# Performance work log

Hardware: AMD Instinct MI355X
Metric: run time of the kernel (lower is better)

The kernel has to match this reference:

```python
import jax, jax.numpy as jnp
import numpy as np

SOS = 1  # parsed_vocab.index('<SOS>')
D = 1024
V_IN = 8000
V_OUT = 8000


def gru_cell(x, h, W_ih, W_hh, b_ih, b_hh):
    # PyTorch GRU cell: gates ordered [r, z, n]
    gi = x @ W_ih.T + b_ih          # [B, 3D]
    gh = h @ W_hh.T + b_hh          # [B, 3D]
    i_r, i_z, i_n = jnp.split(gi, 3, axis=-1)
    h_r, h_z, h_n = jnp.split(gh, 3, axis=-1)
    r = jax.nn.sigmoid(i_r + h_r)
    z = jax.nn.sigmoid(i_z + h_z)
    n = jnp.tanh(i_n + r * h_n)
    return (1.0 - z) * n + z * h


def setup_inputs() -> dict:
    key = jax.random.key(0)
    ks = jax.random.split(key, 16)
    s = 1.0 / np.sqrt(D)
    f = lambda k, shape: jax.random.uniform(k, shape, jnp.float32, -s, s)
    return {
        "src": jax.random.randint(ks[0], (256, 128), 0, V_IN),
        "tgt": jax.random.randint(ks[1], (128, 128), 0, V_OUT),
        "enc_emb": jax.random.normal(ks[2], (V_IN, D), jnp.float32),
        "enc_W_ih": f(ks[3], (3 * D, D)),
        "enc_W_hh": f(ks[4], (3 * D, D)),
        "enc_b_ih": f(ks[5], (3 * D,)),
        "enc_b_hh": f(ks[6], (3 * D,)),
        "dec_emb": jax.random.normal(ks[7], (V_OUT, D), jnp.float32),
        "dec_W_ih": f(ks[8], (3 * D, D)),
        "dec_W_hh": f(ks[9], (3 * D, D)),
        "dec_b_ih": f(ks[10], (3 * D,)),
        "dec_b_hh": f(ks[11], (3 * D,)),
        "out_W": f(ks[12], (V_OUT, D)),
        "out_b": f(ks[13], (V_OUT,)),
    }


def reference(src, tgt, enc_emb, enc_W_ih, enc_W_hh, enc_b_ih, enc_b_hh,
              dec_emb, dec_W_ih, dec_W_hh, dec_b_ih, dec_b_hh, out_W, out_b):
    B = src.shape[1]
    # ---- Encoder: GRU over src, keep final hidden ----
    xs = enc_emb[src]  # [S_src, B, D]
    h0 = jnp.zeros((B, D), xs.dtype)

    def enc_step(h, x):
        return gru_cell(x, h, enc_W_ih, enc_W_hh, enc_b_ih, enc_b_hh), None

    h_enc, _ = jax.lax.scan(enc_step, h0, xs)

    # ---- Decoder: greedy argmax feedback (eval path, tf_ratio=0) ----
    tok0 = jnp.full((B,), SOS, dtype=src.dtype)

    def dec_step(carry, _):
        h, tok = carry
        x = dec_emb[tok]                                  # [B, D]
        h_new = gru_cell(x, h, dec_W_ih, dec_W_hh, dec_b_ih, dec_b_hh)
        logits = h_new @ out_W.T + out_b                  # [B, V_OUT]
        next_tok = jnp.argmax(logits, axis=-1).astype(tok.dtype)
        return (h_new, next_tok), logits

    target_length = tgt.shape[0]
    _, logits = jax.lax.scan(dec_step, (h_enc, tok0), None, length=target_length)
    return logits  # [S_tgt, B, V_OUT]
```

## Files before the change

kernel.cpp:

```cpp
#include <hip/hip_runtime.h>
#include <math.h>

#define DD    1024
#define BB    128
#define G3    3072
#define VOUT  8000
#define S_SRC 256
#define S_TGT 128
#define SOS   1
#define GRID  768
#define KS_F  4

__device__ __forceinline__ float cload(const float* p) {
    return __hip_atomic_load(p, __ATOMIC_RELAXED, __HIP_MEMORY_SCOPE_AGENT);
}
__device__ __forceinline__ void cstore(float* p, float v) {
    __hip_atomic_store(p, v, __ATOMIC_RELAXED, __HIP_MEMORY_SCOPE_AGENT);
}
__device__ __forceinline__ int cloadi(const int* p) {
    return __hip_atomic_load(p, __ATOMIC_RELAXED, __HIP_MEMORY_SCOPE_AGENT);
}
__device__ __forceinline__ void cstorei(int* p, int v) {
    __hip_atomic_store(p, v, __ATOMIC_RELAXED, __HIP_MEMORY_SCOPE_AGENT);
}

__device__ __forceinline__ void gbar(unsigned* bar) {
    __builtin_amdgcn_s_waitcnt(0);
    __syncthreads();
    if (threadIdx.x == 0) {
        unsigned old = __hip_atomic_fetch_add(bar, 1u, __ATOMIC_RELAXED,
                                              __HIP_MEMORY_SCOPE_AGENT);
        unsigned target = (old / GRID + 1u) * GRID;
        while (__hip_atomic_load(bar, __ATOMIC_RELAXED,
                                 __HIP_MEMORY_SCOPE_AGENT) < target)
            __builtin_amdgcn_s_sleep(1);
    }
    __syncthreads();
}

__global__ __launch_bounds__(256) void k_init(float* __restrict__ h, int* __restrict__ tok,
                                              unsigned* __restrict__ bar) {
    int idx = blockIdx.x * 256 + threadIdx.x;
    if (idx < BB * DD) h[idx] = 0.0f;
    if (idx < BB) tok[idx] = SOS;
    if (idx == 0) bar[0] = 0u;
}

template<bool COHA>
__device__ __forceinline__ void gemm_core(
    float (* __restrict__ As)[132], float (* __restrict__ Bs)[34],
    const float* __restrict__ A0, const float* __restrict__ A1,
    const float* __restrict__ A2, const float* __restrict__ A3,
    const float* __restrict__ Brow, int kbeg, int ntiles,
    float (&acc)[8][2])
{
    const int tid = threadIdx.x;
    const int kq  = (tid & 7) * 4;
    const int r0  = tid >> 3;
    const int tx  = tid & 15, ty = tid >> 4;
    const float* Arow[4] = {A0, A1, A2, A3};

    for (int t = 0; t < ntiles; ++t) {
        const int k0 = kbeg + t * 32;
        #pragma unroll
        for (int p = 0; p < 4; ++p) {
            const float* ap = Arow[p] + k0 + kq;
            float vx, vy, vz, vw;
            if (COHA) {
                vx = cload(ap + 0); vy = cload(ap + 1);
                vz = cload(ap + 2); vw = cload(ap + 3);
            } else {
                float4 v = *reinterpret_cast<const float4*>(ap);
                vx = v.x; vy = v.y; vz = v.z; vw = v.w;
            }
            int m = r0 + p * 32;
            As[kq+0][m] = vx; As[kq+1][m] = vy; As[kq+2][m] = vz; As[kq+3][m] = vw;
        }
        {
            float4 v = *reinterpret_cast<const float4*>(Brow + k0 + kq);
            Bs[kq+0][r0] = v.x; Bs[kq+1][r0] = v.y; Bs[kq+2][r0] = v.z; Bs[kq+3][r0] = v.w;
        }
        __syncthreads();
        #pragma unroll
        for (int k = 0; k < 32; ++k) {
            float a[8];
            #pragma unroll
            for (int i = 0; i < 8; ++i) a[i] = As[k][ty*8 + i];
            float b0 = Bs[k][tx*2 + 0], b1 = Bs[k][tx*2 + 1];
            #pragma unroll
            for (int i = 0; i < 8; ++i) {
                acc[i][0] = fmaf(a[i], b0, acc[i][0]);
                acc[i][1] = fmaf(a[i], b1, acc[i][1]);
            }
        }
        __syncthreads();
    }
}


__global__ __launch_bounds__(256, 3) void k_enc_p(
    const float* __restrict__ emb, const int* __restrict__ src,
    const float* __restrict__ Wih, const float* __restrict__ bih,
    const float* __restrict__ Whh, const float* __restrict__ bhh,
    float* __restrict__ h, float* __restrict__ gh_p,
    float* __restrict__ gi_buf, int CH, unsigned* bar)
{
    __shared__ float As[32][132];
    __shared__ float Bs[32][34];
    const int bid = blockIdx.x, tid = threadIdx.x;
    const int r0 = tid >> 3, tx = tid & 15, ty = tid >> 4;

    for (int s = 0; s < S_SRC; ++s) {
        if ((s & (CH - 1)) == 0) {
            const int cs = bid / 96, nt = bid % 96;
            if (cs < CH) {
                const int* srow = src + (s + cs) * BB;
                const float* A0 = emb + (size_t)srow[r0 +  0] * DD;
                const float* A1 = emb + (size_t)srow[r0 + 32] * DD;
                const float* A2 = emb + (size_t)srow[r0 + 64] * DD;
                const float* A3 = emb + (size_t)srow[r0 + 96] * DD;
                float acc[8][2] = {};
                gemm_core<false>(As, Bs, A0, A1, A2, A3,
                                 Wih + (size_t)(nt*32 + r0) * DD, 0, DD/32, acc);
                float* C = gi_buf + (size_t)cs * (BB * G3);
                #pragma unroll
                for (int i = 0; i < 8; ++i) {
                    int m = ty*8 + i;
                    #pragma unroll
                    for (int j = 0; j < 2; ++j) {
                        int n = nt*32 + tx*2 + j;
                        cstore(&C[(size_t)m * G3 + n], acc[i][j] + bih[n]);
                    }
                }
            }
            gbar(bar);
        }
        {
            const int kh = bid / 96, nt = bid % 96;
            const float* A0 = h + (size_t)(r0 +  0) * DD;
            const float* A1 = h + (size_t)(r0 + 32) * DD;
            const float* A2 = h + (size_t)(r0 + 64) * DD;
            const float* A3 = h + (size_t)(r0 + 96) * DD;
            float acc[8][2] = {};
            gemm_core<true>(As, Bs, A0, A1, A2, A3,
                            Whh + (size_t)(nt*32 + r0) * DD, kh * 128, 4, acc);
            float* C = gh_p + (size_t)kh * (BB * G3);
            #pragma unroll
            for (int i = 0; i < 8; ++i) {
                int m = ty*8 + i;
                cstore(&C[(size_t)m * G3 + nt*32 + tx*2 + 0], acc[i][0]);
                cstore(&C[(size_t)m * G3 + nt*32 + tx*2 + 1], acc[i][1]);
            }
        }
        gbar(bar);
        {
            int idx = bid * 256 + tid;
            if (idx < BB * DD) {
                int b = idx >> 10, d = idx & 1023;
                size_t o = (size_t)b * G3 + d;
                const float* gib = gi_buf + (size_t)(s & (CH-1)) * (BB * G3);
                float ir = cload(&gib[o]), iz = cload(&gib[o + DD]),
                      in_ = cload(&gib[o + 2*DD]);
                float hr = bhh[d], hz = bhh[DD + d], hn = bhh[2*DD + d];
                #pragma unroll
                for (int p = 0; p < 8; ++p) {
                    const float* g = gh_p + (size_t)p * (BB * G3);
                    hr += cload(&g[o]); hz += cload(&g[o + DD]); hn += cload(&g[o + 2*DD]);
                }
                float r = 1.0f / (1.0f + expf(-(ir + hr)));
                float z = 1.0f / (1.0f + expf(-(iz + hz)));
                float n = tanhf(in_ + r * hn);
                float hv = cload(&h[idx]);
                cstore(&h[idx], (1.0f - z) * n + z * hv);
            }
        }
        gbar(bar);
    }
}

__global__ __launch_bounds__(256, 3) void k_dec_p(
    const float* __restrict__ emb,
    const float* __restrict__ Wih, const float* __restrict__ bih,
    const float* __restrict__ Whh, const float* __restrict__ bhh,
    const float* __restrict__ outW, const float* __restrict__ outb,
    float* __restrict__ h, float* __restrict__ g_p,
    float* __restrict__ lg_p, int* __restrict__ tok,
    float* __restrict__ out, int KSL, unsigned* bar)
{
    __shared__ float As[32][132];
    __shared__ float Bs[32][34];
    float* sv = &As[0][0];
    int*   si = (int*)&As[8][0];
    const int bid = blockIdx.x, tid = threadIdx.x;
    const int r0 = tid >> 3, tx = tid & 15, ty = tid >> 4;

    for (int t = 0; t < S_TGT; ++t) {
        {
            const int side = bid / 384;
            const int rem  = bid - side * 384;
            const int kh   = rem / 96, nt = rem % 96;
            float acc[8][2] = {};
            if (side) {
                const float* A0 = h + (size_t)(r0 +  0) * DD;
                const float* A1 = h + (size_t)(r0 + 32) * DD;
                const float* A2 = h + (size_t)(r0 + 64) * DD;
                const float* A3 = h + (size_t)(r0 + 96) * DD;
                gemm_core<true>(As, Bs, A0, A1, A2, A3,
                                Whh + (size_t)(nt*32 + r0) * DD, kh * 256, 8, acc);
            } else {
                const float* A0 = emb + (size_t)cloadi(&tok[r0 +  0]) * DD;
                const float* A1 = emb + (size_t)cloadi(&tok[r0 + 32]) * DD;
                const float* A2 = emb + (size_t)cloadi(&tok[r0 + 64]) * DD;
                const float* A3 = emb + (size_t)cloadi(&tok[r0 + 96]) * DD;
                gemm_core<false>(As, Bs, A0, A1, A2, A3,
                                 Wih + (size_t)(nt*32 + r0) * DD, kh * 256, 8, acc);
            }
            float* C = g_p + (size_t)(side*4 + kh) * (BB * G3);
            #pragma unroll
            for (int i = 0; i < 8; ++i) {
                int m = ty*8 + i;
                cstore(&C[(size_t)m * G3 + nt*32 + tx*2 + 0], acc[i][0]);
                cstore(&C[(size_t)m * G3 + nt*32 + tx*2 + 1], acc[i][1]);
            }
        }
        gbar(bar);
        {
            int idx = bid * 256 + tid;
            if (idx < BB * DD) {
                int b = idx >> 10, d = idx & 1023;
                size_t o = (size_t)b * G3 + d;
                float ir = bih[d], iz = bih[DD + d], in_ = bih[2*DD + d];
                #pragma unroll
                for (int p = 0; p < 4; ++p) {
                    const float* g = g_p + (size_t)p * (BB * G3);
                    ir += cload(&g[o]); iz += cload(&g[o + DD]); in_ += cload(&g[o + 2*DD]);
                }
                float hr = bhh[d], hz = bhh[DD + d], hn = bhh[2*DD + d];
                #pragma unroll
                for (int p = 4; p < 8; ++p) {
                    const float* g = g_p + (size_t)p * (BB * G3);
                    hr += cload(&g[o]); hz += cload(&g[o + DD]); hn += cload(&g[o + 2*DD]);
                }
                float r = 1.0f / (1.0f + expf(-(ir + hr)));
                float z = 1.0f / (1.0f + expf(-(iz + hz)));
                float n = tanhf(in_ + r * hn);
                float hv = cload(&h[idx]);
                cstore(&h[idx], (1.0f - z) * n + z * hv);
            }
        }
        gbar(bar);
        {
            const int kh = bid / 250, nt = bid % 250;
            if (kh < KSL) {
                const int t0 = (32 * kh) / KSL, t1 = (32 * (kh + 1)) / KSL;
                const float* A0 = h + (size_t)(r0 +  0) * DD;
                const float* A1 = h + (size_t)(r0 + 32) * DD;
                const float* A2 = h + (size_t)(r0 + 64) * DD;
                const float* A3 = h + (size_t)(r0 + 96) * DD;
                float acc[8][2] = {};
                gemm_core<true>(As, Bs, A0, A1, A2, A3,
                                outW + (size_t)(nt*32 + r0) * DD, t0 * 32, t1 - t0, acc);
                float* C = lg_p + (size_t)kh * (BB * VOUT);
                #pragma unroll
                for (int i = 0; i < 8; ++i) {
                    int m = ty*8 + i;
                    cstore(&C[(size_t)m * VOUT + nt*32 + tx*2 + 0], acc[i][0]);
                    cstore(&C[(size_t)m * VOUT + nt*32 + tx*2 + 1], acc[i][1]);
                }
            }
        }
        gbar(bar);
        if (bid < BB) {
            const int b = bid;
            const size_t ro = (size_t)b * VOUT;
            float* Ct = out + (size_t)t * (BB * VOUT) + ro;
            float bv = -INFINITY; int bi = 0x7fffffff;
            for (int v = tid * 4; v < VOUT; v += 1024) {
                float4 rr = *reinterpret_cast<const float4*>(outb + v);
                for (int kh = 0; kh < KSL; ++kh) {
                    const float* P = lg_p + (size_t)kh * (BB * VOUT) + ro + v;
                    rr.x += cload(P + 0); rr.y += cload(P + 1);
                    rr.z += cload(P + 2); rr.w += cload(P + 3);
                }
                *reinterpret_cast<float4*>(Ct + v) = rr;
                if (rr.x > bv) { bv = rr.x; bi = v + 0; }
                if (rr.y > bv) { bv = rr.y; bi = v + 1; }
                if (rr.z > bv) { bv = rr.z; bi = v + 2; }
                if (rr.w > bv) { bv = rr.w; bi = v + 3; }
            }
            sv[tid] = bv; si[tid] = bi;
            __syncthreads();
            for (int st = 128; st > 0; st >>= 1) {
                if (tid < st) {
                    if (sv[tid+st] > sv[tid] ||
                        (sv[tid+st] == sv[tid] && si[tid+st] < si[tid])) {
                        sv[tid] = sv[tid+st]; si[tid] = si[tid+st];
                    }
                }
                __syncthreads();
            }
            if (tid == 0) cstorei(&tok[b], si[0]);
        }
        gbar(bar);
    }
}


__global__ __launch_bounds__(256) void k_gi_chunk(
    const float* __restrict__ emb, const int* __restrict__ src_c,
    const float* __restrict__ Wih, const float* __restrict__ bih,
    float* __restrict__ gi_buf)
{
    __shared__ float As[32][132];
    __shared__ float Bs[32][34];
    const int n0    = blockIdx.x * 32;
    const int mbase = blockIdx.y * 128;
    const int tid = threadIdx.x;
    const int r0  = tid >> 3, tx = tid & 15, ty = tid >> 4;

    const float* A[4];
    #pragma unroll
    for (int p = 0; p < 4; ++p)
        A[p] = emb + (size_t)src_c[mbase + r0 + p * 32] * DD;
    float acc[8][2] = {};
    gemm_core<false>(As, Bs, A[0], A[1], A[2], A[3],
                     Wih + (size_t)(n0 + r0) * DD, 0, DD/32, acc);
    #pragma unroll
    for (int i = 0; i < 8; ++i) {
        size_t m = (size_t)(mbase + ty*8 + i);
        #pragma unroll
        for (int j = 0; j < 2; ++j) {
            int n = n0 + tx*2 + j;
            gi_buf[m * G3 + n] = acc[i][j] + bih[n];
        }
    }
}

__global__ __launch_bounds__(256) void k_gates_ks(
    const float* __restrict__ emb, const int* __restrict__ tok,
    const float* __restrict__ h,
    const float* __restrict__ Wih, const float* __restrict__ Whh,
    float* __restrict__ gi_base, float* __restrict__ gh_base,
    int side_base)
{
    __shared__ float As[32][132];
    __shared__ float Bs[32][34];
    const int side = side_base + blockIdx.y;
    const int kh   = blockIdx.z;
    const int kseg = DD / KS_F;
    const float* __restrict__ W = side ? Whh : Wih;
    float* __restrict__ C = (side ? gh_base : gi_base) + (size_t)kh * (BB * G3);

    const int n0  = blockIdx.x * 32;
    const int tid = threadIdx.x;
    const int r0  = tid >> 3, tx = tid & 15, ty = tid >> 4;

    const float* A[4];
    #pragma unroll
    for (int p = 0; p < 4; ++p) {
        int m = r0 + p * 32;
        A[p] = side ? (h + (size_t)m * DD) : (emb + (size_t)tok[m] * DD);
    }
    float acc[8][2] = {};
    gemm_core<false>(As, Bs, A[0], A[1], A[2], A[3],
                     W + (size_t)(n0 + r0) * DD, kh * kseg, kseg / 32, acc);
    #pragma unroll
    for (int i = 0; i < 8; ++i) {
        size_t m = (size_t)(ty*8 + i);
        C[m * G3 + n0 + tx*2 + 0] = acc[i][0];
        C[m * G3 + n0 + tx*2 + 1] = acc[i][1];
    }
}

__global__ __launch_bounds__(256) void k_logits_ks(
    const float* __restrict__ h, const float* __restrict__ W,
    float* __restrict__ p_base)
{
    __shared__ float As[32][132];
    __shared__ float Bs[32][34];
    const int kh   = blockIdx.y;
    const int kseg = DD / 2;
    float* __restrict__ C = p_base + (size_t)kh * (BB * VOUT);

    const int n0  = blockIdx.x * 32;
    const int tid = threadIdx.x;
    const int r0  = tid >> 3, tx = tid & 15, ty = tid >> 4;

    const float* A[4];
    #pragma unroll
    for (int p = 0; p < 4; ++p) A[p] = h + (size_t)(r0 + p * 32) * DD;
    float acc[8][2] = {};
    gemm_core<false>(As, Bs, A[0], A[1], A[2], A[3],
                     W + (size_t)(n0 + r0) * DD, kh * kseg, kseg / 32, acc);
    #pragma unroll
    for (int i = 0; i < 8; ++i) {
        size_t m = (size_t)(ty*8 + i);
        C[m * VOUT + n0 + tx*2 + 0] = acc[i][0];
        C[m * VOUT + n0 + tx*2 + 1] = acc[i][1];
    }
}

__global__ __launch_bounds__(256) void k_update_f(
    const float* __restrict__ gi_base, int ns_i, const float* __restrict__ bih,
    const float* __restrict__ gh_base, int ns_h, const float* __restrict__ bhh,
    float* __restrict__ h)
{
    int idx = blockIdx.x * 256 + threadIdx.x;
    int b = idx >> 10, d = idx & 1023;
    size_t o = (size_t)b * G3 + d;

    float ir = 0.f, iz = 0.f, in_ = 0.f;
    for (int p = 0; p < ns_i; ++p) {
        const float* g = gi_base + (size_t)p * (BB * G3);
        ir += g[o]; iz += g[o + DD]; in_ += g[o + 2*DD];
    }
    if (bih) { ir += bih[d]; iz += bih[DD + d]; in_ += bih[2*DD + d]; }

    float hr = 0.f, hz = 0.f, hn = 0.f;
    for (int p = 0; p < ns_h; ++p) {
        const float* g = gh_base + (size_t)p * (BB * G3);
        hr += g[o]; hz += g[o + DD]; hn += g[o + 2*DD];
    }
    hr += bhh[d]; hz += bhh[DD + d]; hn += bhh[2*DD + d];

    float r = 1.0f / (1.0f + expf(-(ir + hr)));
    float z = 1.0f / (1.0f + expf(-(iz + hz)));
    float n = tanhf(in_ + r * hn);
    float hv = h[idx];
    h[idx] = (1.0f - z) * n + z * hv;
}

__global__ __launch_bounds__(256) void k_argmax_out(
    const float* __restrict__ p0, const float* __restrict__ p1,
    const float* __restrict__ bias,
    float* __restrict__ outC, int* __restrict__ tok)
{
    const int b = blockIdx.x;
    const size_t ro = (size_t)b * VOUT;
    const int tid = threadIdx.x;

    float bv = -INFINITY; int bi = 0x7fffffff;
    for (int v = tid * 4; v < VOUT; v += 1024) {
        float4 a = *reinterpret_cast<const float4*>(p0 + ro + v);
        float4 c = *reinterpret_cast<const float4*>(p1 + ro + v);
        float4 bb = *reinterpret_cast<const float4*>(bias + v);
        float4 r;
        r.x = a.x + c.x + bb.x;
        r.y = a.y + c.y + bb.y;
        r.z = a.z + c.z + bb.z;
        r.w = a.w + c.w + bb.w;
        *reinterpret_cast<float4*>(outC + ro + v) = r;
        if (r.x > bv) { bv = r.x; bi = v + 0; }
        if (r.y > bv) { bv = r.y; bi = v + 1; }
        if (r.z > bv) { bv = r.z; bi = v + 2; }
        if (r.w > bv) { bv = r.w; bi = v + 3; }
    }
    __shared__ float sv[256];
    __shared__ int   si[256];
    sv[tid] = bv; si[tid] = bi;
    __syncthreads();
    for (int s = 128; s > 0; s >>= 1) {
        if (tid < s) {
            if (sv[tid+s] > sv[tid] || (sv[tid+s] == sv[tid] && si[tid+s] < si[tid])) {
                sv[tid] = sv[tid+s]; si[tid] = si[tid+s];
            }
        }
        __syncthreads();
    }
    if (tid == 0) tok[b] = si[0];
}

extern "C" void kernel_launch(void* const* d_in, const int* in_sizes, int n_in,
                              void* d_out, int out_size, void* d_ws, size_t ws_size,
                              hipStream_t stream) {
    const int*   src     = (const int*)  d_in[0];
    const float* enc_emb = (const float*)d_in[2];
    const float* eWih    = (const float*)d_in[3];
    const float* eWhh    = (const float*)d_in[4];
    const float* ebih    = (const float*)d_in[5];
    const float* ebhh    = (const float*)d_in[6];
    const float* dec_emb = (const float*)d_in[7];
    const float* dWih    = (const float*)d_in[8];
    const float* dWhh    = (const float*)d_in[9];
    const float* dbih    = (const float*)d_in[10];
    const float* dbhh    = (const float*)d_in[11];
    const float* outW    = (const float*)d_in[12];
    const float* outb    = (const float*)d_in[13];
    float* out = (float*)d_out;

    float* h    = (float*)d_ws;
    float* g_p  = h + BB * DD;
    int*  tok   = (int*)(g_p + 8 * BB * G3);
    unsigned* bar = (unsigned*)(tok + 128);
    float* scratch = (float*)(tok + 256);

    size_t fixed = (size_t)((char*)scratch - (char*)d_ws);
    size_t avail = (ws_size > fixed) ? ws_size - fixed : 0;
    int KSLv = (avail >= (size_t)3 * BB * VOUT * 4) ? 3 : 2;
    int CH = 8;
    while (CH > 1 && (size_t)CH * BB * G3 * 4 > avail) CH >>= 1;

    float* gi_buf = scratch;
    float* lg_p   = scratch;

    static int persist_ok = -1;
    if (persist_ok < 0) {
        int nb_e = 0, nb_d = 0, ncu = 0, dev = 0;
        hipError_t e0 = hipGetDevice(&dev);
        hipError_t e1 = hipOccupancyMaxActiveBlocksPerMultiprocessor(
            &nb_e, (const void*)k_enc_p, 256, 0);
        hipError_t e2 = hipOccupancyMaxActiveBlocksPerMultiprocessor(
            &nb_d, (const void*)k_dec_p, 256, 0);
        hipError_t e3 = hipDeviceGetAttribute(
            &ncu, hipDeviceAttributeMultiprocessorCount, dev);
        persist_ok = (e0 == hipSuccess && e1 == hipSuccess && e2 == hipSuccess &&
                      e3 == hipSuccess && nb_e >= 3 && nb_d >= 3 &&
                      (long)ncu * 3 >= GRID) ? 1 : 0;
    }

    k_init<<<512, 256, 0, stream>>>(h, tok, bar);

    if (persist_ok == 1) {
        k_enc_p<<<GRID, 256, 0, stream>>>(enc_emb, src, eWih, ebih, eWhh, ebhh,
                                          h, g_p, gi_buf, CH, bar);
        k_dec_p<<<GRID, 256, 0, stream>>>(dec_emb, dWih, dbih, dWhh, dbhh,
                                          outW, outb, h, g_p, lg_p, tok,
                                          out, KSLv, bar);
    } else {
        float* gi_p = g_p;
        float* gh_p = g_p + 4 * BB * G3;
        float* p0   = scratch;
        float* p1   = scratch + BB * VOUT;

        for (int c = 0; c < S_SRC; c += CH) {
            k_gi_chunk<<<dim3(96, CH), 256, 0, stream>>>(enc_emb, src + c * BB,
                                                         eWih, ebih, gi_buf);
            for (int s = 0; s < CH; ++s) {
                k_gates_ks<<<dim3(96, 1, KS_F), 256, 0, stream>>>(
                    enc_emb, tok, h, eWih, eWhh, nullptr, gh_p, 1);
                k_update_f<<<512, 256, 0, stream>>>(
                    gi_buf + (size_t)s * BB * G3, 1, nullptr, gh_p, KS_F, ebhh, h);
            }
        }
        for (int t = 0; t < S_TGT; ++t) {
            k_gates_ks<<<dim3(96, 2, KS_F), 256, 0, stream>>>(
                dec_emb, tok, h, dWih, dWhh, gi_p, gh_p, 0);
            k_update_f<<<512, 256, 0, stream>>>(gi_p, KS_F, dbih, gh_p, KS_F, dbhh, h);
            k_logits_ks<<<dim3(250, 2), 256, 0, stream>>>(h, outW, p0);
            float* Ct = out + (size_t)t * BB * VOUT;
            k_argmax_out<<<128, 256, 0, stream>>>(p0, p1, outb, Ct, tok);
        }
    }
}
```

Before: 24.48 ms.

## Use hierarchical grid barrier and register-prefetch the next GEMM tile

Result: slower. 26.08 ms, median of 2 (+6.6%).

```diff
diff --git a/kernel.cpp b/kernel.cpp
--- a/kernel.cpp
+++ b/kernel.cpp
@@ -9,6 +9,8 @@
 #define S_TGT 128
 #define SOS   1
 #define GRID  768
+#define NGRP  8
+#define GSZ   (GRID / NGRP)
 #define KS_F  4
 
 __device__ __forceinline__ float cload(const float* p) {
@@ -24,26 +26,35 @@
     __hip_atomic_store(p, v, __ATOMIC_RELAXED, __HIP_MEMORY_SCOPE_AGENT);
 }
 
-__device__ __forceinline__ void gbar(unsigned* bar) {
+__device__ __forceinline__ void gbar(unsigned* cnt, unsigned* gcnt,
+                                     unsigned* epoch, int grp, unsigned& gen) {
     __builtin_amdgcn_s_waitcnt(0);
     __syncthreads();
     if (threadIdx.x == 0) {
-        unsigned old = __hip_atomic_fetch_add(bar, 1u, __ATOMIC_RELAXED,
-                                              __HIP_MEMORY_SCOPE_AGENT);
-        unsigned target = (old / GRID + 1u) * GRID;
-        while (__hip_atomic_load(bar, __ATOMIC_RELAXED,
-                                 __HIP_MEMORY_SCOPE_AGENT) < target)
-            __builtin_amdgcn_s_sleep(1);
+        const unsigned g = gen;
+        unsigned old = __hip_atomic_fetch_add(&cnt[grp << 5], 1u,
+                          __ATOMIC_RELAXED, __HIP_MEMORY_SCOPE_AGENT);
+        if (old == g * GSZ + (GSZ - 1u)) {
+            unsigned o2 = __hip_atomic_fetch_add(gcnt, 1u,
+                          __ATOMIC_RELAXED, __HIP_MEMORY_SCOPE_AGENT);
+            if (o2 == g * NGRP + (NGRP - 1u))
+                __hip_atomic_store(epoch, g + 1u, __ATOMIC_RELAXED,
+                                   __HIP_MEMORY_SCOPE_AGENT);
+        }
+        while (__hip_atomic_load(epoch, __ATOMIC_RELAXED,
+                                 __HIP_MEMORY_SCOPE_AGENT) < g + 1u)
+            __builtin_amdgcn_s_sleep(2);
     }
     __syncthreads();
+    gen++;
 }
 
 __global__ __launch_bounds__(256) void k_init(float* __restrict__ h, int* __restrict__ tok,
-                                              unsigned* __restrict__ bar) {
+                                              unsigned* __restrict__ barU) {
     int idx = blockIdx.x * 256 + threadIdx.x;
     if (idx < BB * DD) h[idx] = 0.0f;
     if (idx < BB) tok[idx] = SOS;
-    if (idx == 0) bar[0] = 0u;
+    if (idx < 512) barU[idx] = 0u;
 }
 
 template<bool COHA>
@@ -60,27 +71,37 @@
     const int tx  = tid & 15, ty = tid >> 4;
     const float* Arow[4] = {A0, A1, A2, A3};
 
-    for (int t = 0; t < ntiles; ++t) {
+    float va[4][4];
+    float4 vb;
+    auto issue = [&](int t) {
         const int k0 = kbeg + t * 32;
         #pragma unroll
         for (int p = 0; p < 4; ++p) {
             const float* ap = Arow[p] + k0 + kq;
-            float vx, vy, vz, vw;
             if (COHA) {
-                vx = cload(ap + 0); vy = cload(ap + 1);
-                vz = cload(ap + 2); vw = cload(ap + 3);
+                #pragma unroll
+                for (int j = 0; j < 4; ++j) va[p][j] = cload(ap + j);
             } else {
                 float4 v = *reinterpret_cast<const float4*>(ap);
-                vx = v.x; vy = v.y; vz = v.z; vw = v.w;
-            }
+                va[p][0] = v.x; va[p][1] = v.y; va[p][2] = v.z; va[p][3] = v.w;
+            }
+        }
+        vb = *reinterpret_cast<const float4*>(Brow + k0 + kq);
+    };
+
+    issue(0);
+    for (int t = 0; t < ntiles; ++t) {
+        __syncthreads();
+        #pragma unroll
+        for (int p = 0; p < 4; ++p) {
             int m = r0 + p * 32;
-            As[kq+0][m] = vx; As[kq+1][m] = vy; As[kq+2][m] = vz; As[kq+3][m] = vw;
-        }
-        {
-            float4 v = *reinterpret_cast<const float4*>(Brow + k0 + kq);
-            Bs[kq+0][r0] = v.x; Bs[kq+1][r0] = v.y; Bs[kq+2][r0] = v.z; Bs[kq+3][r0] = v.w;
-        }
+            #pragma unroll
+            for (int j = 0; j < 4; ++j) As[kq + j][m] = va[p][j];
+        }
+        Bs[kq+0][r0] = vb.x; Bs[kq+1][r0] = vb.y;
+        Bs[kq+2][r0] = vb.z; Bs[kq+3][r0] = vb.w;
         __syncthreads();
+        if (t + 1 < ntiles) issue(t + 1);
         #pragma unroll
         for (int k = 0; k < 32; ++k) {
             float a[8];
@@ -93,7 +114,6 @@
                 acc[i][1] = fmaf(a[i], b1, acc[i][1]);
             }
         }
-        __syncthreads();
     }
 }
 
@@ -103,12 +123,17 @@
     const float* __restrict__ Wih, const float* __restrict__ bih,
     const float* __restrict__ Whh, const float* __restrict__ bhh,
     float* __restrict__ h, float* __restrict__ gh_p,
-    float* __restrict__ gi_buf, int CH, unsigned* bar)
+    float* __restrict__ gi_buf, int CH, unsigned* barU)
 {
     __shared__ float As[32][132];
     __shared__ float Bs[32][34];
+    unsigned* cnt   = barU;
+    unsigned* gcnt  = barU + 256;
+    unsigned* epoch = barU + 288;
     const int bid = blockIdx.x, tid = threadIdx.x;
+    const int grp = bid & 7;
     const int r0 = tid >> 3, tx = tid & 15, ty = tid >> 4;
+    unsigned gen = 0;
 
     for (int s = 0; s < S_SRC; ++s) {
         if ((s & (CH - 1)) == 0) {
@@ -133,7 +158,7 @@
                     }
                 }
             }
-            gbar(bar);
+            gbar(cnt, gcnt, epoch, grp, gen);
         }
         {
             const int kh = bid / 96, nt = bid % 96;
@@ -152,7 +177,7 @@
                 cstore(&C[(size_t)m * G3 + nt*32 + tx*2 + 1], acc[i][1]);
             }
         }
-        gbar(bar);
+        gbar(cnt, gcnt, epoch, grp, gen);
         {
             int idx = bid * 256 + tid;
             if (idx < BB * DD) {
@@ -174,7 +199,7 @@
                 cstore(&h[idx], (1.0f - z) * n + z * hv);
             }
         }
-        gbar(bar);
+        gbar(cnt, gcnt, epoch, grp, gen);
     }
 }
 
@@ -185,14 +210,19 @@
     const float* __restrict__ outW, const float* __restrict__ outb,
     float* __restrict__ h, float* __restrict__ g_p,
     float* __restrict__ lg_p, int* __restrict__ tok,
-    float* __restrict__ out, int KSL, unsigned* bar)
+    float* __restrict__ out, int KSL, unsigned* barU, unsigned gen0)
 {
     __shared__ float As[32][132];
     __shared__ float Bs[32][34];
     float* sv = &As[0][0];
     int*   si = (int*)&As[8][0];
+    unsigned* cnt   = barU;
+    unsigned* gcnt  = barU + 256;
+    unsigned* epoch = barU + 288;
     const int bid = blockIdx.x, tid = threadIdx.x;
+    const int grp = bid & 7;
     const int r0 = tid >> 3, tx = tid & 15, ty = tid >> 4;
+    unsigned gen = gen0;
 
     for (int t = 0; t < S_TGT; ++t) {
         {
@@ -223,7 +253,7 @@
                 cstore(&C[(size_t)m * G3 + nt*32 + tx*2 + 1], acc[i][1]);
             }
         }
-        gbar(bar);
+        gbar(cnt, gcnt, epoch, grp, gen);
         {
             int idx = bid * 256 + tid;
             if (idx < BB * DD) {
@@ -248,7 +278,7 @@
                 cstore(&h[idx], (1.0f - z) * n + z * hv);
             }
         }
-        gbar(bar);
+        gbar(cnt, gcnt, epoch, grp, gen);
         {
             const int kh = bid / 250, nt = bid % 250;
             if (kh < KSL) {
@@ -269,7 +299,7 @@
                 }
             }
         }
-        gbar(bar);
+        gbar(cnt, gcnt, epoch, grp, gen);
         if (bid < BB) {
             const int b = bid;
             const size_t ro = (size_t)b * VOUT;
@@ -301,7 +331,7 @@
             }
             if (tid == 0) cstorei(&tok[b], si[0]);
         }
-        gbar(bar);
+        gbar(cnt, gcnt, epoch, grp, gen);
     }
 }
 
@@ -491,14 +521,15 @@
     float* h    = (float*)d_ws;
     float* g_p  = h + BB * DD;
     int*  tok   = (int*)(g_p + 8 * BB * G3);
-    unsigned* bar = (unsigned*)(tok + 128);
-    float* scratch = (float*)(tok + 256);
+    unsigned* barU = (unsigned*)(tok + 128);
+    float* scratch = (float*)(barU + 512);
 
     size_t fixed = (size_t)((char*)scratch - (char*)d_ws);
     size_t avail = (ws_size > fixed) ? ws_size - fixed : 0;
     int KSLv = (avail >= (size_t)3 * BB * VOUT * 4) ? 3 : 2;
     int CH = 8;
     while (CH > 1 && (size_t)CH * BB * G3 * 4 > avail) CH >>= 1;
+    unsigned enc_bars = (unsigned)(2 * S_SRC + S_SRC / CH);
 
     float* gi_buf = scratch;
     float* lg_p   = scratch;
@@ -518,14 +549,14 @@
                       (long)ncu * 3 >= GRID) ? 1 : 0;
     }
 
-    k_init<<<512, 256, 0, stream>>>(h, tok, bar);
+    k_init<<<512, 256, 0, stream>>>(h, tok, barU);
 
     if (persist_ok == 1) {
         k_enc_p<<<GRID, 256, 0, stream>>>(enc_emb, src, eWih, ebih, eWhh, ebhh,
-                                          h, g_p, gi_buf, CH, bar);
+                                          h, g_p, gi_buf, CH, barU);
         k_dec_p<<<GRID, 256, 0, stream>>>(dec_emb, dWih, dbih, dWhh, dbhh,
                                           outW, outb, h, g_p, lg_p, tok,
-                                          out, KSLv, bar);
+                                          out, KSLv, barU, enc_bars);
     } else {
         float* gi_p = g_p;
         float* gh_p = g_p + 4 * BB * G3;
```
